# Optimization experiments

Hardware: AMD Instinct MI355X
Metric: run time of the kernel (lower is better)

The kernel has to match this reference:

```python
import jax, jax.numpy as jnp
import numpy as np

B, S, E, NH = 2, 2048, 1024, 4
HD = E // NH  # 256


def setup_inputs() -> dict:
    key = jax.random.key(0)
    ks = jax.random.split(key, 8)
    return {
        "q": jax.random.normal(ks[0], (B, S, E), jnp.float32),
        "k": jax.random.normal(ks[1], (B, S, E), jnp.float32),
        "v": jax.random.normal(ks[2], (B, S, E), jnp.float32),
        # gate Dense params (kernel zero-init in the module; use small random for a nontrivial baseline)
        "igate_kernel": jax.random.normal(ks[3], (3 * E, NH), jnp.float32) * 0.02,
        "igate_bias": jax.random.normal(ks[4], (NH,), jnp.float32) * 0.1,
        "fgate_kernel": jax.random.normal(ks[5], (3 * E, NH), jnp.float32) * 0.02,
        "fgate_bias": jnp.linspace(3.0, 6.0, NH, dtype=jnp.float32),  # bias_linspace_init
        "rms_scale": jax.random.normal(ks[6], (HD,), jnp.float32) * 0.02,
    }


def _mlstm_head(q, k, v, ig, fg, eps=1e-06):
    # q,k,v: (S, DH); ig, fg: (S, 1)
    s, dh = q.shape
    log_f = jax.nn.log_sigmoid(fg)                       # (S,1)
    cs = jnp.concatenate([jnp.zeros((1, 1), log_f.dtype),
                          jnp.cumsum(log_f, axis=0)], axis=0)  # (S+1,1)
    neg = jnp.asarray(-0.7 * jnp.finfo(cs.dtype).max, cs.dtype)
    log_d = jnp.where(jnp.tri(s, dtype=bool),
                      (cs - cs.T)[1:, 1:] + ig.T, neg)   # (S,S)
    m = jnp.max(log_d, axis=-1, keepdims=True)           # row-wise stabilizer
    d = jnp.exp(log_d - m)
    c = (q @ (k.T / jnp.sqrt(dh))) * d                   # (S,S)
    n = jnp.maximum(jnp.sum(c, axis=-1, keepdims=True), jnp.exp(-m))
    return (c / (n + eps)) @ v                           # (S,DH)


def reference(q, k, v, igate_kernel, igate_bias, fgate_kernel, fgate_bias, rms_scale):
    b, s, e = q.shape
    nh = igate_kernel.shape[1]
    hd = e // nh
    gate_in = jnp.concatenate((q, k, v), axis=-1)                 # (B,S,3E)
    ig = (gate_in @ igate_kernel + igate_bias).swapaxes(-1, -2)[..., None]  # (B,NH,S,1)
    fg = (gate_in @ fgate_kernel + fgate_bias).swapaxes(-1, -2)[..., None]  # (B,NH,S,1)
    qh = q.reshape(b, s, nh, hd).swapaxes(1, 2)                   # (B,NH,S,HD)
    kh = k.reshape(b, s, nh, hd).swapaxes(1, 2)
    vh = v.reshape(b, s, nh, hd).swapaxes(1, 2)
    h = jax.vmap(jax.vmap(_mlstm_head))(qh, kh, vh, ig, fg)      # (B,NH,S,HD)
    # RMSNorm over head_dim with (1+scale)
    var = jnp.mean(jnp.square(h.astype(jnp.float32)), axis=-1, keepdims=True)
    h = (h * jax.lax.rsqrt(var + 1e-06)).astype(h.dtype) * (1.0 + rms_scale)
    return h.swapaxes(1, 2).reshape(b, s, e)
```

## Files before the change

kernel.cpp:

```cpp
#include <hip/hip_runtime.h>
#include <math.h>

static constexpr int B_  = 2;
static constexpr int S_  = 2048;
static constexpr int E_  = 1024;
static constexpr int NH_ = 4;
static constexpr int HD_ = 256;
static constexpr int BH_ = B_ * NH_;

typedef __attribute__((ext_vector_type(8))) _Float16 half8;
typedef __attribute__((ext_vector_type(4))) float    f32x4;
typedef __attribute__((ext_vector_type(4))) _Float16 half4v;

__global__ __launch_bounds__(1024) void prep_kernel(
    const float* __restrict__ q, const float* __restrict__ k, const float* __restrict__ v,
    const float* __restrict__ igk, const float* __restrict__ igb,
    const float* __restrict__ fgk, const float* __restrict__ fgb,
    float* __restrict__ ig_out, float* __restrict__ fg_out,
    _Float16* __restrict__ Qh, _Float16* __restrict__ Kh, _Float16* __restrict__ Vt)
{
    __shared__ __align__(16) char PSM[98304];
    float4* wi = (float4*)PSM;
    float4* wf = wi + 3 * E_;

    const int t = threadIdx.x;
    #pragma unroll
    for (int i = 0; i < 3; ++i) {
        int e = t + 1024 * i;
        wi[e] = ((const float4*)igk)[e];
        wf[e] = ((const float4*)fgk)[e];
    }
    __syncthreads();

    const int wave = t >> 6;
    const int l    = t & 63;
    const int bs   = blockIdx.x * 16 + wave;
    const int b = bs >> 11, s = bs & (S_ - 1);
    const float* qrow = q + (size_t)bs * E_;
    const float* krow = k + (size_t)bs * E_;
    const float* vrow = v + (size_t)bs * E_;

    float accI[4] = {0.f,0.f,0.f,0.f}, accF[4] = {0.f,0.f,0.f,0.f};
    #pragma unroll
    for (int j = 0; j < 48; ++j) {
        const int e = l + 64 * j;
        float g;
        if (j < 16)       g = qrow[e];
        else if (j < 32)  g = krow[e - E_];
        else              g = vrow[e - 2 * E_];
        if (j < 16) {
            int hh = e >> 8, d = e & 255;
            Qh[(((size_t)(b * NH_ + hh)) * S_ + s) * HD_ + d] = (_Float16)(g * 0.0625f);
        } else if (j < 32) {
            int e2 = e - E_; int hh = e2 >> 8, d = e2 & 255;
            Kh[(((size_t)(b * NH_ + hh)) * S_ + s) * HD_ + d] = (_Float16)g;
        }
        float4 wiv = wi[e];
        float4 wfv = wf[e];
        accI[0] = fmaf(g, wiv.x, accI[0]); accI[1] = fmaf(g, wiv.y, accI[1]);
        accI[2] = fmaf(g, wiv.z, accI[2]); accI[3] = fmaf(g, wiv.w, accI[3]);
        accF[0] = fmaf(g, wfv.x, accF[0]); accF[1] = fmaf(g, wfv.y, accF[1]);
        accF[2] = fmaf(g, wfv.z, accF[2]); accF[3] = fmaf(g, wfv.w, accF[3]);
    }
    #pragma unroll
    for (int m = 1; m < 64; m <<= 1) {
        #pragma unroll
        for (int h = 0; h < 4; ++h) {
            accI[h] += __shfl_xor(accI[h], m);
            accF[h] += __shfl_xor(accF[h], m);
        }
    }
    if (l == 0) {
        #pragma unroll
        for (int h = 0; h < 4; ++h) {
            ig_out[((size_t)(b * NH_ + h)) * S_ + s] = accI[h] + igb[h];
            fg_out[((size_t)(b * NH_ + h)) * S_ + s] = accF[h] + fgb[h];
        }
    }

    __syncthreads();
    {
        float (*tile)[65] = (float(*)[65])(PSM + (t >> 8) * 16640);
        const int tid = t & 255;
        const int m  = blockIdx.x * 4 + (t >> 8);
        const int bh = m & 7;
        const int sb = (m >> 3) & 31;
        const int db = m >> 8;
        const int bb = bh >> 2, hh = bh & 3;
        const int j4 = (tid & 15) * 4;
        const int i0 = tid >> 4;
        const float* src = v + ((size_t)(bb * S_ + sb * 64)) * E_ + hh * HD_ + db * 64;
        #pragma unroll
        for (int p = 0; p < 4; ++p) {
            int i = i0 + p * 16;
            float4 val = *(const float4*)(src + (size_t)i * E_ + j4);
            tile[i][j4] = val.x; tile[i][j4+1] = val.y; tile[i][j4+2] = val.z; tile[i][j4+3] = val.w;
        }
        __syncthreads();
        const int s4 = (tid & 15) * 4;
        const int d0 = tid >> 4;
        _Float16* dst = Vt + ((size_t)bh * HD_ + db * 64) * S_ + sb * 64;
        #pragma unroll
        for (int p = 0; p < 4; ++p) {
            int d = d0 + p * 16;
            half4v pk;
            pk.x = (_Float16)tile[s4][d];   pk.y = (_Float16)tile[s4+1][d];
            pk.z = (_Float16)tile[s4+2][d]; pk.w = (_Float16)tile[s4+3][d];
            *(half4v*)(dst + (size_t)d * S_ + s4) = pk;
        }
    }
}

static constexpr int KSS = 264;
static constexpr int VSS = 72;
static constexpr int CBS = 265;
static constexpr int OFF_PLS  = 64 * KSS * 2 + 256 * VSS * 2;
static constexpr int OFF_RS2  = OFF_PLS + 4 * 640 * 2;
static constexpr int OFF_AMM  = OFF_RS2 + 128;
static constexpr int OFF_G    = OFF_AMM + S_ * 4;
static constexpr int OFF_M    = OFF_G   + S_ * 4;
static constexpr int SMB      = OFF_M   + S_ * 4;

__global__ __launch_bounds__(256, 1) void mlstm_kernel(
    const _Float16* __restrict__ Qh, const _Float16* __restrict__ Kh,
    const _Float16* __restrict__ Vt,
    const float* __restrict__ ig, const float* __restrict__ fg,
    const float* __restrict__ rms_scale, float* __restrict__ out)
{
    __shared__ __align__(16) char SMEM[SMB];
    _Float16* Ks    = (_Float16*)SMEM;
    _Float16* Vs    = (_Float16*)(SMEM + 64 * KSS * 2);
    float*    comb  = (float*)SMEM;
    float*    rsum2 = (float*)(SMEM + OFF_RS2);
    float*    sAmM  = (float*)(SMEM + OFF_AMM);
    float*    sG    = (float*)(SMEM + OFF_G);
    float*    sM    = (float*)(SMEM + OFF_M);
    _Float16* Pls   = (_Float16*)(SMEM + OFF_PLS);

    const int z  = blockIdx.x;
    const int bh = z & 7;
    const int u  = z >> 3;
    const int b  = bh >> 2, h = bh & 3;
    const int t  = threadIdx.x;
    const int w  = t >> 6;
    const int l  = t & 63;
    const int col  = l & 15;
    const int quad = l >> 4;
    const int qo   = quad * 8;
    const int rw   = w & 1;
    const int cw   = w >> 1;

    {
        float* sc = (float*)SMEM;
        const float* fgp = fg + (size_t)bh * S_;
        const float* igp = ig + (size_t)bh * S_;
        float ls[8];
        float run = 0.f;
        #pragma unroll
        for (int i = 0; i < 8; ++i) {
            float x = fgp[t * 8 + i];
            float lg = (x >= 0.f) ? -log1pf(expf(-x)) : (x - log1pf(expf(x)));
            run += lg;
            ls[i] = run;
        }
        sc[t] = run;
        __syncthreads();
        for (int off = 1; off < 256; off <<= 1) {
            float vv = (t >= off) ? sc[t - off] : 0.f;
            __syncthreads();
            sc[t] += vv;
            __syncthreads();
        }
        float excl = sc[t] - run;
        float A[8], g[8], gm[8];
        #pragma unroll
        for (int i = 0; i < 8; ++i) A[i] = excl + ls[i];
        float rmax = -__builtin_inff();
        #pragma unroll
        for (int i = 0; i < 8; ++i) {
            g[i] = igp[t * 8 + i] - A[i];
            rmax = fmaxf(rmax, g[i]);
            gm[i] = rmax;
        }
        __syncthreads();
        sc[t] = rmax;
        __syncthreads();
        for (int off = 1; off < 256; off <<= 1) {
            float vv = (t >= off) ? sc[t - off] : -__builtin_inff();
            __syncthreads();
            sc[t] = fmaxf(sc[t], vv);
            __syncthreads();
        }
        float exm = (t == 0) ? -__builtin_inff() : sc[t - 1];
        #pragma unroll
        for (int i = 0; i < 8; ++i) {
            float cm = fmaxf(exm, gm[i]);
            float Mi = A[i] + cm;
            sAmM[t * 8 + i] = A[i] - Mi;
            sG[t * 8 + i]   = g[i];
            sM[t * 8 + i]   = Mi;
        }
        __syncthreads();
    }

    const _Float16* Qp  = Qh + (size_t)bh * S_ * HD_;
    const _Float16* Kp  = Kh + (size_t)bh * S_ * HD_;
    const _Float16* Vtp = Vt + (size_t)bh * HD_ * S_;
    _Float16* Pw = Pls + w * 640;

    half8 kpre[8], vpre[8];
    auto issueK = [&](int c0n) {
        #pragma unroll
        for (int i = 0; i < 8; ++i) {
            int p = t + 256 * i;
            int row = p >> 5, ck = p & 31;
            kpre[i] = *(const half8*)(Kp + (size_t)(c0n + row) * HD_ + ck * 8);
        }
    };
    auto issueV = [&](int c0n) {
        #pragma unroll
        for (int i = 0; i < 8; ++i) {
            int p = t + 256 * i;
            int n = p >> 3, ch = p & 7;
            vpre[i] = *(const half8*)(Vtp + (size_t)n * S_ + c0n + ch * 8);
        }
    };

    issueK(0);
    issueV(0);

    for (int pass = 0; pass < 2; ++pass) {
        const int rb = pass ? (63 - u) : u;
        const int rowbase = rb * 32 + rw * 16;

        half8 qf[8];
        #pragma unroll
        for (int kk = 0; kk < 8; ++kk)
            qf[kk] = *(const half8*)(Qp + (size_t)(rowbase + col) * HD_ + kk * 32 + qo);
        float amM[4];
        #pragma unroll
        for (int rr = 0; rr < 4; ++rr) amM[rr] = sAmM[rowbase + quad * 4 + rr];

        f32x4 acc[16];
        #pragma unroll
        for (int nn = 0; nn < 16; ++nn) acc[nn] = (f32x4){0.f, 0.f, 0.f, 0.f};
        float rs[4] = {0.f, 0.f, 0.f, 0.f};

        const int Tt = (rb >> 1) + 1;
        for (int jt = 0; jt < Tt; ++jt) {
            const int c0 = jt << 6;
            __syncthreads();
            #pragma unroll
            for (int i = 0; i < 8; ++i) {
                int p = t + 256 * i;
                int row = p >> 5, ck = p & 31;
                *(half8*)(Ks + row * KSS + ck * 8) = kpre[i];
            }
            #pragma unroll
            for (int i = 0; i < 8; ++i) {
                int p = t + 256 * i;
                int n = p >> 3, ch = p & 7;
                *(half8*)(Vs + n * VSS + ch * 8) = vpre[i];
            }
            __syncthreads();
            if (!(pass == 1 && jt + 1 == Tt)) {
                const int cn = (jt + 1 < Tt) ? (c0 + 64) : 0;
                issueK(cn);
                issueV(cn);
            }
            const float gv0 = sG[c0 + cw * 32 + col];
            const float gv1 = sG[c0 + cw * 32 + 16 + col];
            f32x4 sc0 = (f32x4){0.f,0.f,0.f,0.f};
            f32x4 sc1 = (f32x4){0.f,0.f,0.f,0.f};
            #pragma unroll
            for (int kk = 0; kk < 8; ++kk) {
                half8 kf0 = *(const half8*)(Ks + (cw * 32 + col) * KSS + kk * 32 + qo);
                half8 kf1 = *(const half8*)(Ks + (cw * 32 + 16 + col) * KSS + kk * 32 + qo);
                sc0 = __builtin_amdgcn_mfma_f32_16x16x32_f16(qf[kk], kf0, sc0, 0, 0, 0);
                sc1 = __builtin_amdgcn_mfma_f32_16x16x32_f16(qf[kk], kf1, sc1, 0, 0, 0);
            }
            #pragma unroll
            for (int rr = 0; rr < 4; ++rr) {
                const int ig_ = rowbase + quad * 4 + rr;
                float e0 = __expf(amM[rr] + gv0);
                float e1 = __expf(amM[rr] + gv1);
                float p0 = (c0 + cw * 32 + col      <= ig_) ? sc0[rr] * e0 : 0.f;
                float p1 = (c0 + cw * 32 + 16 + col <= ig_) ? sc1[rr] * e1 : 0.f;
                rs[rr] += p0 + p1;
                Pw[(quad * 4 + rr) * 40 + col]      = (_Float16)p0;
                Pw[(quad * 4 + rr) * 40 + 16 + col] = (_Float16)p1;
            }
            half8 af = *(const half8*)(Pw + col * 40 + qo);
            #pragma unroll
            for (int nn = 0; nn < 16; ++nn) {
                half8 vf = *(const half8*)(Vs + (nn * 16 + col) * VSS + cw * 32 + qo);
                acc[nn] = __builtin_amdgcn_mfma_f32_16x16x32_f16(af, vf, acc[nn], 0, 0, 0);
            }
        }

        #pragma unroll
        for (int m = 1; m < 16; m <<= 1) {
            #pragma unroll
            for (int rr = 0; rr < 4; ++rr) rs[rr] += __shfl_xor(rs[rr], m);
        }
        __syncthreads();
        if (w >= 2) {
            if (col == 0) {
                #pragma unroll
                for (int rr = 0; rr < 4; ++rr) rsum2[rw * 16 + quad * 4 + rr] = rs[rr];
            }
            #pragma unroll
            for (int nn = 0; nn < 16; ++nn)
                #pragma unroll
                for (int rr = 0; rr < 4; ++rr)
                    comb[(rw * 16 + quad * 4 + rr) * CBS + nn * 16 + col] = acc[nn][rr];
        }
        __syncthreads();
        if (w < 2) {
            float inv[4], ss[4];
            #pragma unroll
            for (int rr = 0; rr < 4; ++rr) {
                float tot = rs[rr] + rsum2[rw * 16 + quad * 4 + rr];
                float Mv = sM[rowbase + quad * 4 + rr];
                float n = fmaxf(tot, __expf(-Mv)) + 1e-6f;
                inv[rr] = 1.0f / n;
                ss[rr] = 0.f;
            }
            #pragma unroll
            for (int nn = 0; nn < 16; ++nn) {
                #pragma unroll
                for (int rr = 0; rr < 4; ++rr) {
                    float hv = (acc[nn][rr] +
                                comb[(rw * 16 + quad * 4 + rr) * CBS + nn * 16 + col]) * inv[rr];
                    acc[nn][rr] = hv;
                    ss[rr] = fmaf(hv, hv, ss[rr]);
                }
            }
            #pragma unroll
            for (int m = 1; m < 16; m <<= 1) {
                #pragma unroll
                for (int rr = 0; rr < 4; ++rr) ss[rr] += __shfl_xor(ss[rr], m);
            }
            #pragma unroll
            for (int rr = 0; rr < 4; ++rr) {
                float rstd = rsqrtf(ss[rr] * (1.0f / HD_) + 1e-6f);
                float* orow = out + ((size_t)(b * S_ + rowbase + quad * 4 + rr)) * E_ + h * HD_;
                #pragma unroll
                for (int nn = 0; nn < 16; ++nn)
                    orow[nn * 16 + col] = acc[nn][rr] * rstd * (1.0f + rms_scale[nn * 16 + col]);
            }
        }
        __syncthreads();
    }
}

extern "C" void kernel_launch(void* const* d_in, const int* in_sizes, int n_in,
                              void* d_out, int out_size, void* d_ws, size_t ws_size,
                              hipStream_t stream) {
    (void)in_sizes; (void)n_in; (void)out_size; (void)ws_size;
    const float* q   = (const float*)d_in[0];
    const float* k   = (const float*)d_in[1];
    const float* v   = (const float*)d_in[2];
    const float* igk = (const float*)d_in[3];
    const float* igb = (const float*)d_in[4];
    const float* fgk = (const float*)d_in[5];
    const float* fgb = (const float*)d_in[6];
    const float* rsc = (const float*)d_in[7];
    float* out = (float*)d_out;

    float* ws  = (float*)d_ws;
    float* ig  = ws;
    float* fg  = ws + (size_t)BH_ * S_;
    _Float16* Qh = (_Float16*)(ws + (size_t)2 * BH_ * S_);
    _Float16* Kh = Qh + (size_t)BH_ * S_ * HD_;
    _Float16* Vt = Kh + (size_t)BH_ * S_ * HD_;

    prep_kernel<<<B_ * S_ / 16, 1024, 0, stream>>>(q, k, v, igk, igb, fgk, fgb,
                                                   ig, fg, Qh, Kh, Vt);
    mlstm_kernel<<<BH_ * 32, 256, 0, stream>>>(Qh, Kh, Vt, ig, fg, rsc, out);
}
```

Baseline: 186.4 us.

## Split mLSTM block into 8 waves partitioning output columns instead of key columns

Raises the attention block from 4 to 8 waves. Each wave now owns one 16-key slice of the score tile and a 64-wide slice of the head dimension, where before it owned 32 keys and the full 256-wide output. The P tile is shared through LDS with an extra barrier, and row sums and RMS sums are combined across waves via small LDS arrays. This removes the cross-wave accumulator reduction through LDS and cuts per-thread accumulator registers so more waves can be resident. The cost is an extra barrier per key tile and more redundant Q-fragment loads.

```diff
diff --git a/kernel.cpp b/kernel.cpp
--- a/kernel.cpp
+++ b/kernel.cpp
@@ -113,15 +113,17 @@
 
 static constexpr int KSS = 264;
 static constexpr int VSS = 72;
-static constexpr int CBS = 265;
-static constexpr int OFF_PLS  = 64 * KSS * 2 + 256 * VSS * 2;
-static constexpr int OFF_RS2  = OFF_PLS + 4 * 640 * 2;
-static constexpr int OFF_AMM  = OFF_RS2 + 128;
-static constexpr int OFF_G    = OFF_AMM + S_ * 4;
-static constexpr int OFF_M    = OFF_G   + S_ * 4;
-static constexpr int SMB      = OFF_M   + S_ * 4;
-
-__global__ __launch_bounds__(256, 1) void mlstm_kernel(
+static constexpr int PBS = 72;
+static constexpr int OFF_VS  = 64 * KSS * 2;
+static constexpr int OFF_PB  = OFF_VS + 256 * VSS * 2;
+static constexpr int OFF_RSE = OFF_PB + 2 * 16 * PBS * 2;
+static constexpr int OFF_SSE = OFF_RSE + 512;
+static constexpr int OFF_AMM = OFF_SSE + 512;
+static constexpr int OFF_G   = OFF_AMM + S_ * 4;
+static constexpr int OFF_M   = OFF_G   + S_ * 4;
+static constexpr int SMB     = OFF_M   + S_ * 4;
+
+__global__ __launch_bounds__(512, 2) void mlstm_kernel(
     const _Float16* __restrict__ Qh, const _Float16* __restrict__ Kh,
     const _Float16* __restrict__ Vt,
     const float* __restrict__ ig, const float* __restrict__ fg,
@@ -129,13 +131,13 @@
 {
     __shared__ __align__(16) char SMEM[SMB];
     _Float16* Ks    = (_Float16*)SMEM;
-    _Float16* Vs    = (_Float16*)(SMEM + 64 * KSS * 2);
-    float*    comb  = (float*)SMEM;
-    float*    rsum2 = (float*)(SMEM + OFF_RS2);
+    _Float16* Vs    = (_Float16*)(SMEM + OFF_VS);
+    _Float16* Pb    = (_Float16*)(SMEM + OFF_PB);
+    float*    rsumE = (float*)(SMEM + OFF_RSE);
+    float*    ssE   = (float*)(SMEM + OFF_SSE);
     float*    sAmM  = (float*)(SMEM + OFF_AMM);
     float*    sG    = (float*)(SMEM + OFF_G);
     float*    sM    = (float*)(SMEM + OFF_M);
-    _Float16* Pls   = (_Float16*)(SMEM + OFF_PLS);
 
     const int z  = blockIdx.x;
     const int bh = z & 7;
@@ -147,45 +149,45 @@
     const int col  = l & 15;
     const int quad = l >> 4;
     const int qo   = quad * 8;
-    const int rw   = w & 1;
-    const int cw   = w >> 1;
+    const int rw   = w >> 2;
+    const int cq   = w & 3;
 
     {
         float* sc = (float*)SMEM;
         const float* fgp = fg + (size_t)bh * S_;
         const float* igp = ig + (size_t)bh * S_;
-        float ls[8];
+        float ls[4];
         float run = 0.f;
         #pragma unroll
-        for (int i = 0; i < 8; ++i) {
-            float x = fgp[t * 8 + i];
+        for (int i = 0; i < 4; ++i) {
+            float x = fgp[t * 4 + i];
             float lg = (x >= 0.f) ? -log1pf(expf(-x)) : (x - log1pf(expf(x)));
             run += lg;
             ls[i] = run;
         }
         sc[t] = run;
         __syncthreads();
-        for (int off = 1; off < 256; off <<= 1) {
+        for (int off = 1; off < 512; off <<= 1) {
             float vv = (t >= off) ? sc[t - off] : 0.f;
             __syncthreads();
             sc[t] += vv;
             __syncthreads();
         }
         float excl = sc[t] - run;
-        float A[8], g[8], gm[8];
-        #pragma unroll
-        for (int i = 0; i < 8; ++i) A[i] = excl + ls[i];
+        float A[4], g[4], gm[4];
+        #pragma unroll
+        for (int i = 0; i < 4; ++i) A[i] = excl + ls[i];
         float rmax = -__builtin_inff();
         #pragma unroll
-        for (int i = 0; i < 8; ++i) {
-            g[i] = igp[t * 8 + i] - A[i];
+        for (int i = 0; i < 4; ++i) {
+            g[i] = igp[t * 4 + i] - A[i];
             rmax = fmaxf(rmax, g[i]);
             gm[i] = rmax;
         }
         __syncthreads();
         sc[t] = rmax;
         __syncthreads();
-        for (int off = 1; off < 256; off <<= 1) {
+        for (int off = 1; off < 512; off <<= 1) {
             float vv = (t >= off) ? sc[t - off] : -__builtin_inff();
             __syncthreads();
             sc[t] = fmaxf(sc[t], vv);
@@ -193,12 +195,12 @@
         }
         float exm = (t == 0) ? -__builtin_inff() : sc[t - 1];
         #pragma unroll
-        for (int i = 0; i < 8; ++i) {
+        for (int i = 0; i < 4; ++i) {
             float cm = fmaxf(exm, gm[i]);
             float Mi = A[i] + cm;
-            sAmM[t * 8 + i] = A[i] - Mi;
-            sG[t * 8 + i]   = g[i];
-            sM[t * 8 + i]   = Mi;
+            sAmM[t * 4 + i] = A[i] - Mi;
+            sG[t * 4 + i]   = g[i];
+            sM[t * 4 + i]   = Mi;
         }
         __syncthreads();
     }
@@ -206,21 +208,21 @@
     const _Float16* Qp  = Qh + (size_t)bh * S_ * HD_;
     const _Float16* Kp  = Kh + (size_t)bh * S_ * HD_;
     const _Float16* Vtp = Vt + (size_t)bh * HD_ * S_;
-    _Float16* Pw = Pls + w * 640;
-
-    half8 kpre[8], vpre[8];
+    _Float16* Pbr = Pb + rw * 16 * PBS;
+
+    half8 kpre[4], vpre[4];
     auto issueK = [&](int c0n) {
         #pragma unroll
-        for (int i = 0; i < 8; ++i) {
-            int p = t + 256 * i;
+        for (int i = 0; i < 4; ++i) {
+            int p = t + 512 * i;
             int row = p >> 5, ck = p & 31;
             kpre[i] = *(const half8*)(Kp + (size_t)(c0n + row) * HD_ + ck * 8);
         }
     };
     auto issueV = [&](int c0n) {
         #pragma unroll
-        for (int i = 0; i < 8; ++i) {
-            int p = t + 256 * i;
+        for (int i = 0; i < 4; ++i) {
+            int p = t + 512 * i;
             int n = p >> 3, ch = p & 7;
             vpre[i] = *(const half8*)(Vtp + (size_t)n * S_ + c0n + ch * 8);
         }
@@ -241,9 +243,9 @@
         #pragma unroll
         for (int rr = 0; rr < 4; ++rr) amM[rr] = sAmM[rowbase + quad * 4 + rr];
 
-        f32x4 acc[16];
-        #pragma unroll
-        for (int nn = 0; nn < 16; ++nn) acc[nn] = (f32x4){0.f, 0.f, 0.f, 0.f};
+        f32x4 acc[4];
+        #pragma unroll
+        for (int nn = 0; nn < 4; ++nn) acc[nn] = (f32x4){0.f, 0.f, 0.f, 0.f};
         float rs[4] = {0.f, 0.f, 0.f, 0.f};
 
         const int Tt = (rb >> 1) + 1;
@@ -251,14 +253,14 @@
             const int c0 = jt << 6;
             __syncthreads();
             #pragma unroll
-            for (int i = 0; i < 8; ++i) {
-                int p = t + 256 * i;
+            for (int i = 0; i < 4; ++i) {
+                int p = t + 512 * i;
                 int row = p >> 5, ck = p & 31;
                 *(half8*)(Ks + row * KSS + ck * 8) = kpre[i];
             }
             #pragma unroll
-            for (int i = 0; i < 8; ++i) {
-                int p = t + 256 * i;
+            for (int i = 0; i < 4; ++i) {
+                int p = t + 512 * i;
                 int n = p >> 3, ch = p & 7;
                 *(half8*)(Vs + n * VSS + ch * 8) = vpre[i];
             }
@@ -268,33 +270,31 @@
                 issueK(cn);
                 issueV(cn);
             }
-            const float gv0 = sG[c0 + cw * 32 + col];
-            const float gv1 = sG[c0 + cw * 32 + 16 + col];
+            const float gv = sG[c0 + cq * 16 + col];
             f32x4 sc0 = (f32x4){0.f,0.f,0.f,0.f};
-            f32x4 sc1 = (f32x4){0.f,0.f,0.f,0.f};
             #pragma unroll
             for (int kk = 0; kk < 8; ++kk) {
-                half8 kf0 = *(const half8*)(Ks + (cw * 32 + col) * KSS + kk * 32 + qo);
-                half8 kf1 = *(const half8*)(Ks + (cw * 32 + 16 + col) * KSS + kk * 32 + qo);
-                sc0 = __builtin_amdgcn_mfma_f32_16x16x32_f16(qf[kk], kf0, sc0, 0, 0, 0);
-                sc1 = __builtin_amdgcn_mfma_f32_16x16x32_f16(qf[kk], kf1, sc1, 0, 0, 0);
+                half8 kf = *(const half8*)(Ks + (cq * 16 + col) * KSS + kk * 32 + qo);
+                sc0 = __builtin_amdgcn_mfma_f32_16x16x32_f16(qf[kk], kf, sc0, 0, 0, 0);
             }
             #pragma unroll
             for (int rr = 0; rr < 4; ++rr) {
                 const int ig_ = rowbase + quad * 4 + rr;
-                float e0 = __expf(amM[rr] + gv0);
-                float e1 = __expf(amM[rr] + gv1);
-                float p0 = (c0 + cw * 32 + col      <= ig_) ? sc0[rr] * e0 : 0.f;
-                float p1 = (c0 + cw * 32 + 16 + col <= ig_) ? sc1[rr] * e1 : 0.f;
-                rs[rr] += p0 + p1;
-                Pw[(quad * 4 + rr) * 40 + col]      = (_Float16)p0;
-                Pw[(quad * 4 + rr) * 40 + 16 + col] = (_Float16)p1;
-            }
-            half8 af = *(const half8*)(Pw + col * 40 + qo);
-            #pragma unroll
-            for (int nn = 0; nn < 16; ++nn) {
-                half8 vf = *(const half8*)(Vs + (nn * 16 + col) * VSS + cw * 32 + qo);
-                acc[nn] = __builtin_amdgcn_mfma_f32_16x16x32_f16(af, vf, acc[nn], 0, 0, 0);
+                float e0 = __expf(amM[rr] + gv);
+                float p0 = (c0 + cq * 16 + col <= ig_) ? sc0[rr] * e0 : 0.f;
+                rs[rr] += p0;
+                Pbr[(quad * 4 + rr) * PBS + cq * 16 + col] = (_Float16)p0;
+            }
+            __syncthreads();
+            half8 af0 = *(const half8*)(Pbr + col * PBS + qo);
+            half8 af1 = *(const half8*)(Pbr + col * PBS + 32 + qo);
+            #pragma unroll
+            for (int nn = 0; nn < 4; ++nn) {
+                const int n = cq * 64 + nn * 16 + col;
+                half8 vf0 = *(const half8*)(Vs + n * VSS + qo);
+                half8 vf1 = *(const half8*)(Vs + n * VSS + 32 + qo);
+                acc[nn] = __builtin_amdgcn_mfma_f32_16x16x32_f16(af0, vf0, acc[nn], 0, 0, 0);
+                acc[nn] = __builtin_amdgcn_mfma_f32_16x16x32_f16(af1, vf1, acc[nn], 0, 0, 0);
             }
         }
 
@@ -303,51 +303,54 @@
             #pragma unroll
             for (int rr = 0; rr < 4; ++rr) rs[rr] += __shfl_xor(rs[rr], m);
         }
-        __syncthreads();
-        if (w >= 2) {
-            if (col == 0) {
-                #pragma unroll
-                for (int rr = 0; rr < 4; ++rr) rsum2[rw * 16 + quad * 4 + rr] = rs[rr];
-            }
-            #pragma unroll
-            for (int nn = 0; nn < 16; ++nn)
-                #pragma unroll
-                for (int rr = 0; rr < 4; ++rr)
-                    comb[(rw * 16 + quad * 4 + rr) * CBS + nn * 16 + col] = acc[nn][rr];
-        }
-        __syncthreads();
-        if (w < 2) {
-            float inv[4], ss[4];
+        if (col == 0) {
+            #pragma unroll
+            for (int rr = 0; rr < 4; ++rr)
+                rsumE[rw * 64 + cq * 16 + quad * 4 + rr] = rs[rr];
+        }
+        __syncthreads();
+        float inv[4], ss[4];
+        #pragma unroll
+        for (int rr = 0; rr < 4; ++rr) {
+            const int r = quad * 4 + rr;
+            float tot = rsumE[rw * 64 + r] + rsumE[rw * 64 + 16 + r]
+                      + rsumE[rw * 64 + 32 + r] + rsumE[rw * 64 + 48 + r];
+            float Mv = sM[rowbase + r];
+            float n = fmaxf(tot, __expf(-Mv)) + 1e-6f;
+            inv[rr] = 1.0f / n;
+            ss[rr] = 0.f;
+        }
+        #pragma unroll
+        for (int nn = 0; nn < 4; ++nn) {
             #pragma unroll
             for (int rr = 0; rr < 4; ++rr) {
-                float tot = rs[rr] + rsum2[rw * 16 + quad * 4 + rr];
-                float Mv = sM[rowbase + quad * 4 + rr];
-                float n = fmaxf(tot, __expf(-Mv)) + 1e-6f;
-                inv[rr] = 1.0f / n;
-                ss[rr] = 0.f;
-            }
-            #pragma unroll
-            for (int nn = 0; nn < 16; ++nn) {
-                #pragma unroll
-                for (int rr = 0; rr < 4; ++rr) {
-                    float hv = (acc[nn][rr] +
-                                comb[(rw * 16 + quad * 4 + rr) * CBS + nn * 16 + col]) * inv[rr];
-                    acc[nn][rr] = hv;
-                    ss[rr] = fmaf(hv, hv, ss[rr]);
-                }
-            }
-            #pragma unroll
-            for (int m = 1; m < 16; m <<= 1) {
-                #pragma unroll
-                for (int rr = 0; rr < 4; ++rr) ss[rr] += __shfl_xor(ss[rr], m);
-            }
-            #pragma unroll
-            for (int rr = 0; rr < 4; ++rr) {
-                float rstd = rsqrtf(ss[rr] * (1.0f / HD_) + 1e-6f);
-                float* orow = out + ((size_t)(b * S_ + rowbase + quad * 4 + rr)) * E_ + h * HD_;
-                #pragma unroll
-                for (int nn = 0; nn < 16; ++nn)
-                    orow[nn * 16 + col] = acc[nn][rr] * rstd * (1.0f + rms_scale[nn * 16 + col]);
+                float hv = acc[nn][rr] * inv[rr];
+                acc[nn][rr] = hv;
+                ss[rr] = fmaf(hv, hv, ss[rr]);
+            }
+        }
+        #pragma unroll
+        for (int m = 1; m < 16; m <<= 1) {
+            #pragma unroll
+            for (int rr = 0; rr < 4; ++rr) ss[rr] += __shfl_xor(ss[rr], m);
+        }
+        if (col == 0) {
+            #pragma unroll
+            for (int rr = 0; rr < 4; ++rr)
+                ssE[rw * 64 + cq * 16 + quad * 4 + rr] = ss[rr];
+        }
+        __syncthreads();
+        #pragma unroll
+        for (int rr = 0; rr < 4; ++rr) {
+            const int r = quad * 4 + rr;
+            float sst = ssE[rw * 64 + r] + ssE[rw * 64 + 16 + r]
+                      + ssE[rw * 64 + 32 + r] + ssE[rw * 64 + 48 + r];
+            float rstd = rsqrtf(sst * (1.0f / HD_) + 1e-6f);
+            float* orow = out + ((size_t)(b * S_ + rowbase + r)) * E_ + h * HD_;
+            #pragma unroll
+            for (int nn = 0; nn < 4; ++nn) {
+                const int c = cq * 64 + nn * 16 + col;
+                orow[c] = acc[nn][rr] * rstd * (1.0f + rms_scale[c]);
             }
         }
         __syncthreads();
@@ -377,5 +380,5 @@
 
     prep_kernel<<<B_ * S_ / 16, 1024, 0, stream>>>(q, k, v, igk, igb, fgk, fgb,
                                                    ig, fg, Qh, Kh, Vt);
-    mlstm_kernel<<<BH_ * 32, 256, 0, stream>>>(Qh, Kh, Vt, ig, fg, rsc, out);
+    mlstm_kernel<<<BH_ * 32, 512, 0, stream>>>(Qh, Kh, Vt, ig, fg, rsc, out);
 }
```

Measured after the change: 168.5 us. -9.6%, faster.
